# Performance work log

Measured on AMD Instinct MI355X. Metric: run time of the kernel, lower is better.

Reference implementation:

```python
import jax, jax.numpy as jnp
import numpy as np

N_NODES = 50000
N_EDGES = 500000
D_IN = 128
D_HID = 128
D_OUT = 128
N_GRAPHS = 1024


def gcn_conv(x, W, b, row, col, n_nodes):
    # x: [N, d_in] -> [N, d_out]; PyG GCNConv with add_self_loops + symmetric norm
    h = x @ W  # [N, d_out]
    loops = jnp.arange(n_nodes, dtype=row.dtype)
    r = jnp.concatenate([row, loops])  # source
    c = jnp.concatenate([col, loops])  # target
    deg = jax.ops.segment_sum(jnp.ones(r.shape[0], dtype=x.dtype), c, num_segments=n_nodes)
    dinv = jnp.where(deg > 0, jax.lax.rsqrt(jnp.maximum(deg, 1.0)), 0.0)
    norm = dinv[r] * dinv[c]  # [E+N]
    msg = h[r] * norm[:, None]  # gather + scale
    out = jax.ops.segment_sum(msg, c, num_segments=n_nodes)  # scatter-add at targets
    return out + b


def setup_inputs() -> dict:
    key = jax.random.key(0)
    ks = jax.random.split(key, 10)
    x = jax.random.normal(ks[0], (N_NODES, D_IN), dtype=jnp.float32)
    edge_index = jax.random.randint(ks[1], (2, N_EDGES), 0, N_NODES, dtype=jnp.int64)
    batch = jnp.sort(jax.random.randint(ks[2], (N_NODES,), 0, N_GRAPHS, dtype=jnp.int64))
    s1 = 1.0 / np.sqrt(D_IN)
    s2 = 1.0 / np.sqrt(D_HID)
    W1 = jax.random.uniform(ks[3], (D_IN, D_HID), jnp.float32, -s1, s1)
    b1 = jnp.zeros((D_HID,), jnp.float32)
    W2 = jax.random.uniform(ks[4], (D_HID, D_HID), jnp.float32, -s2, s2)
    b2 = jnp.zeros((D_HID,), jnp.float32)
    Wf = jax.random.uniform(ks[5], (D_HID, D_OUT), jnp.float32, -s2, s2)
    bf = jax.random.uniform(ks[6], (D_OUT,), jnp.float32, -s2, s2)
    return {"x": x, "edge_index": edge_index, "batch": batch,
            "W1": W1, "b1": b1, "W2": W2, "b2": b2, "Wf": Wf, "bf": bf}


def reference(x, edge_index, batch, W1, b1, W2, b2, Wf, bf):
    n = x.shape[0]
    row, col = edge_index[0], edge_index[1]
    h = jax.nn.relu(gcn_conv(x, W1, b1, row, col, n))
    h = jax.nn.relu(gcn_conv(h, W2, b2, row, col, n))
    # global_mean_pool over graph ids
    sums = jax.ops.segment_sum(h, batch, num_segments=N_GRAPHS)  # [G, d]
    cnts = jax.ops.segment_sum(jnp.ones((n,), h.dtype), batch, num_segments=N_GRAPHS)
    pooled = sums / jnp.maximum(cnts, 1.0)[:, None]
    return pooled @ Wf + bf  # [G, D_OUT]
```

## Files before the change

### kernel.cpp

```cpp
#include <hip/hip_runtime.h>
#include <hip/hip_bf16.h>


#define D 128

typedef __attribute__((ext_vector_type(8))) short short8;
typedef __attribute__((ext_vector_type(4))) float f32x4;

__device__ __forceinline__ int swz(int row, int kbyte) {
    return row * 256 + (kbyte ^ ((row & 7) << 4));
}

__global__ __launch_bounds__(256) void k_init(int4* __restrict__ degcnt4, int n4, int zb,
                                              const float* __restrict__ W1,
                                              const float* __restrict__ W2,
                                              ushort* __restrict__ h1, ushort* __restrict__ l1,
                                              ushort* __restrict__ h2, ushort* __restrict__ l2) {
    int b = blockIdx.x;
    if (b < zb) {
        int i = b * 256 + threadIdx.x;
        if (i < n4) degcnt4[i] = make_int4(0, 0, 0, 0);
        return;
    }
    int bb = b - zb;
    const float* W = (bb < 8) ? W1 : W2;
    ushort* Wh = (bb < 8) ? h1 : h2;
    ushort* Wl = (bb < 8) ? l1 : l2;
    int t = (bb & 7) * 256 + threadIdx.x;
    int nrow = t >> 4;
    int kc = t & 15;
    uint hw[8], lw[8];
#pragma unroll
    for (int j = 0; j < 8; ++j) {
        float f = W[(kc * 8 + j) * D + nrow];
        uint ub = __float_as_uint(f);
        uint hb = ub & 0xffff0000u;
        float r = f - __uint_as_float(hb);
        hw[j] = hb >> 16;
        lw[j] = __float_as_uint(r) >> 16;
    }
    uint4 vh = make_uint4(hw[0] | (hw[1] << 16), hw[2] | (hw[3] << 16),
                          hw[4] | (hw[5] << 16), hw[6] | (hw[7] << 16));
    uint4 vl = make_uint4(lw[0] | (lw[1] << 16), lw[2] | (lw[3] << 16),
                          lw[4] | (lw[5] << 16), lw[6] | (lw[7] << 16));
    *(uint4*)&Wh[nrow * D + kc * 8] = vh;
    *(uint4*)&Wl[nrow * D + kc * 8] = vl;
}

__global__ void k_deg(const int* __restrict__ col, int* __restrict__ cnt, int E) {
    int e = (blockIdx.x * blockDim.x + threadIdx.x) * 2;
    if (e + 1 < E) {
        int2 c = *(const int2*)&col[e];
        atomicAdd(&cnt[c.x], 1);
        atomicAdd(&cnt[c.y], 1);
    } else if (e < E) {
        atomicAdd(&cnt[col[e]], 1);
    }
}

__global__ __launch_bounds__(256) void k_scan_partial(const int* __restrict__ cnt,
                                                      int* __restrict__ partial, int n) {
    int t = threadIdx.x;
    int base = blockIdx.x * 1024 + t * 4;
    int s = 0;
#pragma unroll
    for (int j = 0; j < 4; ++j) {
        int i = base + j;
        if (i < n) s += cnt[i];
    }
#pragma unroll
    for (int o = 32; o > 0; o >>= 1) s += __shfl_down(s, o, 64);
    __shared__ int ws[4];
    if ((t & 63) == 0) ws[t >> 6] = s;
    __syncthreads();
    if (t == 0) partial[blockIdx.x] = ws[0] + ws[1] + ws[2] + ws[3];
}

__global__ __launch_bounds__(256) void k_scan_final(const int* __restrict__ cnt,
                                                    const int* __restrict__ partial,
                                                    int* __restrict__ offs,
                                                    int* __restrict__ cursor,
                                                    float* __restrict__ dinv,
                                                    int n, int E) {
    int t = threadIdx.x;
    int lane = t & 63;
    int base = blockIdx.x * 1024 + t * 4;
    int v[4];
    int s = 0;
#pragma unroll
    for (int j = 0; j < 4; ++j) {
        int i = base + j;
        v[j] = (i < n) ? cnt[i] : 0;
        s += v[j];
    }
    int inc = s;
#pragma unroll
    for (int o = 1; o < 64; o <<= 1) {
        int u = __shfl_up(inc, o, 64);
        if (lane >= o) inc += u;
    }
    __shared__ int wsum[4];
    __shared__ int bpref;
    if (lane == 63) wsum[t >> 6] = inc;
    if (t == 0) {
        int run = 0;
        for (int b = 0; b < blockIdx.x; ++b) run += partial[b];
        bpref = run;
        if (blockIdx.x == 0) offs[n] = E;
    }
    __syncthreads();
    int woff = 0;
    int w = t >> 6;
    for (int k = 0; k < w; ++k) woff += wsum[k];
    int excl = woff + (inc - s) + bpref;
#pragma unroll
    for (int j = 0; j < 4; ++j) {
        int i = base + j;
        if (i < n) {
            offs[i] = excl;
            cursor[i] = excl;
            dinv[i] = 1.0f / sqrtf((float)(v[j] + 1));
        }
        excl += v[j];
    }
}

__global__ void k_fill(const int* __restrict__ ei, int* __restrict__ cursor,
                       int* __restrict__ csr, int E) {
    int e = (blockIdx.x * blockDim.x + threadIdx.x) * 2;
    if (e + 1 < E) {
        int2 r = *(const int2*)&ei[e];
        int2 c = *(const int2*)&ei[E + e];
        int p0 = atomicAdd(&cursor[c.x], 1);
        csr[p0] = r.x;
        int p1 = atomicAdd(&cursor[c.y], 1);
        csr[p1] = r.y;
    } else if (e < E) {
        int r = ei[e];
        int c = ei[E + e];
        int pos = atomicAdd(&cursor[c], 1);
        csr[pos] = r;
    }
}

#define TM 128
template <bool ASLICED>
__global__ __launch_bounds__(512, 4) void k_gemm(const float* __restrict__ A,
                                                 const ushort* __restrict__ Bt_hi,
                                                 const ushort* __restrict__ Bt_lo,
                                                 const float* __restrict__ dinv,
                                                 float* __restrict__ C, int n) {
    extern __shared__ char lds[];
    char* Bh = lds;
    char* Bl = lds + 32 * 1024;

    int tid = threadIdx.x;
    int wave = tid >> 6, lane = tid & 63;
    int li = lane & 15, lg = lane >> 4;
    int row0 = blockIdx.x * TM;
    int grow = row0 + wave * 16 + li;
    bool valid = grow < n;

    float4 a[4][2];
#pragma unroll
    for (int ks = 0; ks < 4; ++ks) {
        int k0 = ks * 32 + lg * 8;
        if (valid) {
            const float4* p;
            if (ASLICED)
                p = (const float4*)(A + ((size_t)(k0 >> 4) * n + grow) * 16 + (k0 & 15));
            else
                p = (const float4*)(A + (size_t)grow * D + k0);
            a[ks][0] = p[0];
            a[ks][1] = p[1];
        } else {
            a[ks][0] = make_float4(0.f, 0.f, 0.f, 0.f);
            a[ks][1] = make_float4(0.f, 0.f, 0.f, 0.f);
        }
    }

#pragma unroll
    for (int it = tid; it < 2048; it += 512) {
        int r = it >> 4, kc = it & 15;
        uint4 vh = *(const uint4*)(Bt_hi + r * D + kc * 8);
        uint4 vl = *(const uint4*)(Bt_lo + r * D + kc * 8);
        *(uint4*)(Bh + swz(r, kc * 16)) = vh;
        *(uint4*)(Bl + swz(r, kc * 16)) = vl;
    }
    __syncthreads();

    short8 ah[4], al[4];
#pragma unroll
    for (int ks = 0; ks < 4; ++ks) {
        float f[8] = {a[ks][0].x, a[ks][0].y, a[ks][0].z, a[ks][0].w,
                      a[ks][1].x, a[ks][1].y, a[ks][1].z, a[ks][1].w};
#pragma unroll
        for (int j = 0; j < 8; ++j) {
            uint ub = __float_as_uint(f[j]);
            uint hb = ub & 0xffff0000u;
            float r = f[j] - __uint_as_float(hb);
            ah[ks][j] = (short)(hb >> 16);
            al[ks][j] = (short)(__float_as_uint(r) >> 16);
        }
    }

    f32x4 acc[8];
#pragma unroll
    for (int i = 0; i < 8; ++i) acc[i] = (f32x4){0.f, 0.f, 0.f, 0.f};

#pragma unroll
    for (int ks = 0; ks < 4; ++ks) {
        int kb = ks * 64 + lg * 16;
#pragma unroll
        for (int nt = 0; nt < 8; ++nt) {
            short8 bh = *(const short8*)(Bh + swz(nt * 16 + li, kb));
            short8 bl = *(const short8*)(Bl + swz(nt * 16 + li, kb));
            acc[nt] = __builtin_amdgcn_mfma_f32_16x16x32_bf16(ah[ks], bh, acc[nt], 0, 0, 0);
            acc[nt] = __builtin_amdgcn_mfma_f32_16x16x32_bf16(al[ks], bh, acc[nt], 0, 0, 0);
            acc[nt] = __builtin_amdgcn_mfma_f32_16x16x32_bf16(ah[ks], bl, acc[nt], 0, 0, 0);
        }
    }

    int crow0 = row0 + wave * 16 + lg * 4;
#pragma unroll
    for (int j = 0; j < 4; ++j) {
        int gr = crow0 + j;
        if (gr < n) {
            float dv = dinv[gr];
#pragma unroll
            for (int nt = 0; nt < 8; ++nt)
                C[((size_t)nt * n + gr) * 16 + li] = acc[nt][j] * dv;
        }
    }
}

#define AGG_NB 64
__global__ __launch_bounds__(256) void k_agg(const float* __restrict__ hs,
                                             const float* __restrict__ dinv,
                                             const int* __restrict__ offs,
                                             const int* __restrict__ csr,
                                             const float* __restrict__ bias,
                                             float* __restrict__ outs, int n) {
    int slice = blockIdx.x & 7;
    int chunk = blockIdx.x >> 3;
    int node = chunk * AGG_NB + (threadIdx.x >> 2);
    if (node >= n) return;
    int l4 = (threadIdx.x & 3) * 4;

    const float* hbase = hs + (size_t)slice * n * 16;
    float di = dinv[node];
    int s = offs[node], e = offs[node + 1];
    f32x4 acc = *(const f32x4*)(hbase + (size_t)node * 16 + l4);
    int p = s;
    for (; p + 8 <= e; p += 8) {
        int r0 = csr[p],     r1 = csr[p + 1], r2 = csr[p + 2], r3 = csr[p + 3];
        int r4 = csr[p + 4], r5 = csr[p + 5], r6 = csr[p + 6], r7 = csr[p + 7];
        f32x4 h0 = *(const f32x4*)(hbase + (size_t)r0 * 16 + l4);
        f32x4 h1 = *(const f32x4*)(hbase + (size_t)r1 * 16 + l4);
        f32x4 h2 = *(const f32x4*)(hbase + (size_t)r2 * 16 + l4);
        f32x4 h3 = *(const f32x4*)(hbase + (size_t)r3 * 16 + l4);
        f32x4 h4 = *(const f32x4*)(hbase + (size_t)r4 * 16 + l4);
        f32x4 h5 = *(const f32x4*)(hbase + (size_t)r5 * 16 + l4);
        f32x4 h6 = *(const f32x4*)(hbase + (size_t)r6 * 16 + l4);
        f32x4 h7 = *(const f32x4*)(hbase + (size_t)r7 * 16 + l4);
        acc += ((h0 + h1) + (h2 + h3)) + ((h4 + h5) + (h6 + h7));
    }
    for (; p + 4 <= e; p += 4) {
        int r0 = csr[p], r1 = csr[p + 1], r2 = csr[p + 2], r3 = csr[p + 3];
        f32x4 h0 = *(const f32x4*)(hbase + (size_t)r0 * 16 + l4);
        f32x4 h1 = *(const f32x4*)(hbase + (size_t)r1 * 16 + l4);
        f32x4 h2 = *(const f32x4*)(hbase + (size_t)r2 * 16 + l4);
        f32x4 h3 = *(const f32x4*)(hbase + (size_t)r3 * 16 + l4);
        acc += (h0 + h1) + (h2 + h3);
    }
    for (; p < e; ++p) {
        int r = csr[p];
        acc += *(const f32x4*)(hbase + (size_t)r * 16 + l4);
    }
    f32x4 b4 = *(const f32x4*)(bias + slice * 16 + l4);
    f32x4 v;
#pragma unroll
    for (int j = 0; j < 4; ++j) v[j] = fmaxf(acc[j] * di + b4[j], 0.f);
    __builtin_nontemporal_store(v, (f32x4*)(outs + ((size_t)slice * n + node) * 16 + l4));
}

__global__ __launch_bounds__(128) void k_poolfinal(const float* __restrict__ hs,
                                                   const int* __restrict__ batch, int n,
                                                   const float* __restrict__ Wf,
                                                   const float* __restrict__ bf,
                                                   float* __restrict__ out) {
    int g = blockIdx.x;
    int lo = 0, hi = n;
    while (lo < hi) { int m = (lo + hi) >> 1; if (batch[m] < g) lo = m + 1; else hi = m; }
    int s = lo;
    lo = s; hi = n;
    while (lo < hi) { int m = (lo + hi) >> 1; if (batch[m] < g + 1) lo = m + 1; else hi = m; }
    int e = lo;

    int d = threadIdx.x;
    const float* base = hs + (size_t)(d >> 4) * n * 16 + (d & 15);
    float a0 = 0.f, a1 = 0.f, a2 = 0.f, a3 = 0.f;
    int i = s;
    for (; i + 4 <= e; i += 4) {
        a0 += base[(size_t)i * 16];
        a1 += base[(size_t)(i + 1) * 16];
        a2 += base[(size_t)(i + 2) * 16];
        a3 += base[(size_t)(i + 3) * 16];
    }
    for (; i < e; ++i) a0 += base[(size_t)i * 16];
    float acc = (a0 + a1) + (a2 + a3);
    float cnt = (float)(e - s);
    if (cnt < 1.f) cnt = 1.f;

    __shared__ float pr[D];
    pr[d] = acc / cnt;
    __syncthreads();
    float o = bf[d];
#pragma unroll 8
    for (int k = 0; k < D; ++k) o += pr[k] * Wf[k * D + d];
    out[g * D + d] = o;
}

extern "C" void kernel_launch(void* const* d_in, const int* in_sizes, int n_in,
                              void* d_out, int out_size, void* d_ws, size_t ws_size,
                              hipStream_t stream) {
    const float* x  = (const float*)d_in[0];
    const int*   ei = (const int*)d_in[1];
    const int*   bt = (const int*)d_in[2];
    const float* W1 = (const float*)d_in[3];
    const float* b1 = (const float*)d_in[4];
    const float* W2 = (const float*)d_in[5];
    const float* b2 = (const float*)d_in[6];
    const float* Wf = (const float*)d_in[7];
    const float* bf = (const float*)d_in[8];
    float* out = (float*)d_out;

    int n = in_sizes[2];
    int E = in_sizes[1] / 2;
    int G = out_size / D;

    char* w = (char*)d_ws;
    size_t off = 0;
    auto alloc = [&](size_t bytes) -> void* {
        void* p = w + off;
        off = (off + bytes + 511) & ~(size_t)511;
        return p;
    };
    int*    degcnt = (int*)alloc((size_t)n * 4);
    int*    cursor = (int*)alloc((size_t)n * 4);
    int*    offs   = (int*)alloc((size_t)(n + 1) * 4);
    float*  dinv   = (float*)alloc((size_t)n * 4);
    int*    csr    = (int*)alloc((size_t)E * 4);
    float*  hw     = (float*)alloc((size_t)n * D * 4);
    float*  ha     = (float*)alloc((size_t)n * D * 4);
    int*    partial= (int*)alloc((size_t)256 * 4);
    ushort* wt1h   = (ushort*)alloc((size_t)D * D * 2);
    ushort* wt1l   = (ushort*)alloc((size_t)D * D * 2);
    ushort* wt2h   = (ushort*)alloc((size_t)D * D * 2);
    ushort* wt2l   = (ushort*)alloc((size_t)D * D * 2);

    int n4 = (n + 3) / 4;
    int zb = (n4 + 255) / 256;
    k_init<<<zb + 16, 256, 0, stream>>>((int4*)degcnt, n4, zb,
                                        W1, W2, wt1h, wt1l, wt2h, wt2l);

    int e2b = (E / 2 + 255) / 256 + 1;
    int sb = (n + 1023) / 1024;
    k_deg<<<e2b, 256, 0, stream>>>(ei + E, degcnt, E);
    k_scan_partial<<<sb, 256, 0, stream>>>(degcnt, partial, n);
    k_scan_final<<<sb, 256, 0, stream>>>(degcnt, partial, offs, cursor, dinv, n, E);
    k_fill<<<e2b, 256, 0, stream>>>(ei, cursor, csr, E);

    int gb = (n + TM - 1) / TM;
    int ab = 8 * ((n + AGG_NB - 1) / AGG_NB);
    size_t lds_bytes = 64 * 1024;

    k_gemm<false><<<gb, 512, lds_bytes, stream>>>(x, wt1h, wt1l, dinv, hw, n);
    k_agg<<<ab, 256, 0, stream>>>(hw, dinv, offs, csr, b1, ha, n);
    k_gemm<true><<<gb, 512, lds_bytes, stream>>>(ha, wt2h, wt2l, dinv, hw, n);
    k_agg<<<ab, 256, 0, stream>>>(hw, dinv, offs, csr, b2, ha, n);
    k_poolfinal<<<G, 128, 0, stream>>>(ha, bt, n, Wf, bf, out);
}
```

Baseline: 172.9 us.

## Stage CSR slices in LDS for aggregation, widen edge kernels, parallelize pooling

The aggregation kernel now loads each block's offsets and neighbor index range into shared memory once, so the 8 feature-slice blocks no longer each read neighbor indices from global memory per thread. It falls back to global reads when the span exceeds the LDS capacity. The degree and CSR-fill kernels process four edges per thread with int4 loads and issue their atomics together. Pooling splits the binary searches across two threads and reads rows with vector loads spread over four row groups, reduced through shared memory. The cost is extra syncs and LDS use in aggregation.

```diff
diff --git a/kernel.cpp b/kernel.cpp
--- a/kernel.cpp
+++ b/kernel.cpp
@@ -48,13 +48,15 @@
 }
 
 __global__ void k_deg(const int* __restrict__ col, int* __restrict__ cnt, int E) {
-    int e = (blockIdx.x * blockDim.x + threadIdx.x) * 2;
-    if (e + 1 < E) {
-        int2 c = *(const int2*)&col[e];
+    int e = (blockIdx.x * blockDim.x + threadIdx.x) * 4;
+    if (e + 3 < E) {
+        int4 c = *(const int4*)&col[e];
         atomicAdd(&cnt[c.x], 1);
         atomicAdd(&cnt[c.y], 1);
-    } else if (e < E) {
-        atomicAdd(&cnt[col[e]], 1);
+        atomicAdd(&cnt[c.z], 1);
+        atomicAdd(&cnt[c.w], 1);
+    } else {
+        for (; e < E; ++e) atomicAdd(&cnt[col[e]], 1);
     }
 }
 
@@ -127,19 +129,24 @@
 
 __global__ void k_fill(const int* __restrict__ ei, int* __restrict__ cursor,
                        int* __restrict__ csr, int E) {
-    int e = (blockIdx.x * blockDim.x + threadIdx.x) * 2;
-    if (e + 1 < E) {
-        int2 r = *(const int2*)&ei[e];
-        int2 c = *(const int2*)&ei[E + e];
+    int e = (blockIdx.x * blockDim.x + threadIdx.x) * 4;
+    if (e + 3 < E) {
+        int4 r = *(const int4*)&ei[e];
+        int4 c = *(const int4*)&ei[E + e];
         int p0 = atomicAdd(&cursor[c.x], 1);
+        int p1 = atomicAdd(&cursor[c.y], 1);
+        int p2 = atomicAdd(&cursor[c.z], 1);
+        int p3 = atomicAdd(&cursor[c.w], 1);
         csr[p0] = r.x;
-        int p1 = atomicAdd(&cursor[c.y], 1);
         csr[p1] = r.y;
-    } else if (e < E) {
-        int r = ei[e];
-        int c = ei[E + e];
-        int pos = atomicAdd(&cursor[c], 1);
-        csr[pos] = r;
+        csr[p2] = r.z;
+        csr[p3] = r.w;
+    } else {
+        for (; e < E; ++e) {
+            int rr = ei[e], cc = ei[E + e];
+            int pos = atomicAdd(&cursor[cc], 1);
+            csr[pos] = rr;
+        }
     }
 }
 
@@ -235,47 +242,77 @@
 }
 
 #define AGG_NB 64
+#define CSR_CAP 1152
 __global__ __launch_bounds__(256) void k_agg(const float* __restrict__ hs,
                                              const float* __restrict__ dinv,
                                              const int* __restrict__ offs,
                                              const int* __restrict__ csr,
                                              const float* __restrict__ bias,
                                              float* __restrict__ outs, int n) {
+    __shared__ int lofs[AGG_NB + 1];
+    __shared__ int lcsr[CSR_CAP];
     int slice = blockIdx.x & 7;
     int chunk = blockIdx.x >> 3;
-    int node = chunk * AGG_NB + (threadIdx.x >> 2);
+    int node0 = chunk * AGG_NB;
+    int nend = node0 + AGG_NB; if (nend > n) nend = n;
+    int nn = nend - node0;
+    if (threadIdx.x <= nn) lofs[threadIdx.x] = offs[node0 + threadIdx.x];
+    __syncthreads();
+    int S = lofs[0];
+    int span = lofs[nn] - S;
+    bool uselds = (span <= CSR_CAP);
+    if (uselds) {
+        for (int i = threadIdx.x; i < span; i += 256) lcsr[i] = csr[S + i];
+    }
+    __syncthreads();
+
+    int lnode = threadIdx.x >> 2;
+    int node = node0 + lnode;
     if (node >= n) return;
     int l4 = (threadIdx.x & 3) * 4;
 
     const float* hbase = hs + (size_t)slice * n * 16;
     float di = dinv[node];
-    int s = offs[node], e = offs[node + 1];
+    int s = lofs[lnode] - S, e = lofs[lnode + 1] - S;
     f32x4 acc = *(const f32x4*)(hbase + (size_t)node * 16 + l4);
-    int p = s;
-    for (; p + 8 <= e; p += 8) {
-        int r0 = csr[p],     r1 = csr[p + 1], r2 = csr[p + 2], r3 = csr[p + 3];
-        int r4 = csr[p + 4], r5 = csr[p + 5], r6 = csr[p + 6], r7 = csr[p + 7];
-        f32x4 h0 = *(const f32x4*)(hbase + (size_t)r0 * 16 + l4);
-        f32x4 h1 = *(const f32x4*)(hbase + (size_t)r1 * 16 + l4);
-        f32x4 h2 = *(const f32x4*)(hbase + (size_t)r2 * 16 + l4);
-        f32x4 h3 = *(const f32x4*)(hbase + (size_t)r3 * 16 + l4);
-        f32x4 h4 = *(const f32x4*)(hbase + (size_t)r4 * 16 + l4);
-        f32x4 h5 = *(const f32x4*)(hbase + (size_t)r5 * 16 + l4);
-        f32x4 h6 = *(const f32x4*)(hbase + (size_t)r6 * 16 + l4);
-        f32x4 h7 = *(const f32x4*)(hbase + (size_t)r7 * 16 + l4);
-        acc += ((h0 + h1) + (h2 + h3)) + ((h4 + h5) + (h6 + h7));
-    }
-    for (; p + 4 <= e; p += 4) {
-        int r0 = csr[p], r1 = csr[p + 1], r2 = csr[p + 2], r3 = csr[p + 3];
-        f32x4 h0 = *(const f32x4*)(hbase + (size_t)r0 * 16 + l4);
-        f32x4 h1 = *(const f32x4*)(hbase + (size_t)r1 * 16 + l4);
-        f32x4 h2 = *(const f32x4*)(hbase + (size_t)r2 * 16 + l4);
-        f32x4 h3 = *(const f32x4*)(hbase + (size_t)r3 * 16 + l4);
-        acc += (h0 + h1) + (h2 + h3);
-    }
-    for (; p < e; ++p) {
-        int r = csr[p];
-        acc += *(const f32x4*)(hbase + (size_t)r * 16 + l4);
+    if (uselds) {
+        int p = s;
+        for (; p + 8 <= e; p += 8) {
+            int r0 = lcsr[p],     r1 = lcsr[p + 1], r2 = lcsr[p + 2], r3 = lcsr[p + 3];
+            int r4 = lcsr[p + 4], r5 = lcsr[p + 5], r6 = lcsr[p + 6], r7 = lcsr[p + 7];
+            f32x4 h0 = *(const f32x4*)(hbase + (size_t)r0 * 16 + l4);
+            f32x4 h1 = *(const f32x4*)(hbase + (size_t)r1 * 16 + l4);
+            f32x4 h2 = *(const f32x4*)(hbase + (size_t)r2 * 16 + l4);
+            f32x4 h3 = *(const f32x4*)(hbase + (size_t)r3 * 16 + l4);
+            f32x4 h4 = *(const f32x4*)(hbase + (size_t)r4 * 16 + l4);
+            f32x4 h5 = *(const f32x4*)(hbase + (size_t)r5 * 16 + l4);
+            f32x4 h6 = *(const f32x4*)(hbase + (size_t)r6 * 16 + l4);
+            f32x4 h7 = *(const f32x4*)(hbase + (size_t)r7 * 16 + l4);
+            acc += ((h0 + h1) + (h2 + h3)) + ((h4 + h5) + (h6 + h7));
+        }
+        for (; p + 4 <= e; p += 4) {
+            int r0 = lcsr[p], r1 = lcsr[p + 1], r2 = lcsr[p + 2], r3 = lcsr[p + 3];
+            f32x4 h0 = *(const f32x4*)(hbase + (size_t)r0 * 16 + l4);
+            f32x4 h1 = *(const f32x4*)(hbase + (size_t)r1 * 16 + l4);
+            f32x4 h2 = *(const f32x4*)(hbase + (size_t)r2 * 16 + l4);
+            f32x4 h3 = *(const f32x4*)(hbase + (size_t)r3 * 16 + l4);
+            acc += (h0 + h1) + (h2 + h3);
+        }
+        for (; p < e; ++p)
+            acc += *(const f32x4*)(hbase + (size_t)lcsr[p] * 16 + l4);
+    } else {
+        const int* gcsr = csr + S;
+        int p = s;
+        for (; p + 4 <= e; p += 4) {
+            int r0 = gcsr[p], r1 = gcsr[p + 1], r2 = gcsr[p + 2], r3 = gcsr[p + 3];
+            f32x4 h0 = *(const f32x4*)(hbase + (size_t)r0 * 16 + l4);
+            f32x4 h1 = *(const f32x4*)(hbase + (size_t)r1 * 16 + l4);
+            f32x4 h2 = *(const f32x4*)(hbase + (size_t)r2 * 16 + l4);
+            f32x4 h3 = *(const f32x4*)(hbase + (size_t)r3 * 16 + l4);
+            acc += (h0 + h1) + (h2 + h3);
+        }
+        for (; p < e; ++p)
+            acc += *(const f32x4*)(hbase + (size_t)gcsr[p] * 16 + l4);
     }
     f32x4 b4 = *(const f32x4*)(bias + slice * 16 + l4);
     f32x4 v;
@@ -289,32 +326,42 @@
                                                    const float* __restrict__ Wf,
                                                    const float* __restrict__ bf,
                                                    float* __restrict__ out) {
+    __shared__ int sse[2];
     int g = blockIdx.x;
-    int lo = 0, hi = n;
-    while (lo < hi) { int m = (lo + hi) >> 1; if (batch[m] < g) lo = m + 1; else hi = m; }
-    int s = lo;
-    lo = s; hi = n;
-    while (lo < hi) { int m = (lo + hi) >> 1; if (batch[m] < g + 1) lo = m + 1; else hi = m; }
-    int e = lo;
-
+    if (threadIdx.x == 0) {
+        int lo = 0, hi = n;
+        while (lo < hi) { int m = (lo + hi) >> 1; if (batch[m] < g) lo = m + 1; else hi = m; }
+        sse[0] = lo;
+    } else if (threadIdx.x == 64) {
+        int lo = 0, hi = n;
+        while (lo < hi) { int m = (lo + hi) >> 1; if (batch[m] < g + 1) lo = m + 1; else hi = m; }
+        sse[1] = lo;
+    }
+    __syncthreads();
+    int s = sse[0], e = sse[1];
+
+    int q = threadIdx.x & 31;
+    int r = threadIdx.x >> 5;
+    int slice = q >> 2;
+    int l4 = (q & 3) * 4;
+    const float* base = hs + (size_t)slice * n * 16 + l4;
+    f32x4 acc = (f32x4){0.f, 0.f, 0.f, 0.f};
+    for (int i = s + r; i < e; i += 4)
+        acc += *(const f32x4*)(base + (size_t)i * 16);
+
+    __shared__ f32x4 red[128];
+    __shared__ float pr[D];
+    red[threadIdx.x] = acc;
+    __syncthreads();
+    if (threadIdx.x < 32) {
+        f32x4 t = (red[q] + red[q + 32]) + (red[q + 64] + red[q + 96]);
+        float cnt = (float)(e - s);
+        if (cnt < 1.f) cnt = 1.f;
+#pragma unroll
+        for (int j = 0; j < 4; ++j) pr[q * 4 + j] = t[j] / cnt;
+    }
+    __syncthreads();
     int d = threadIdx.x;
-    const float* base = hs + (size_t)(d >> 4) * n * 16 + (d & 15);
-    float a0 = 0.f, a1 = 0.f, a2 = 0.f, a3 = 0.f;
-    int i = s;
-    for (; i + 4 <= e; i += 4) {
-        a0 += base[(size_t)i * 16];
-        a1 += base[(size_t)(i + 1) * 16];
-        a2 += base[(size_t)(i + 2) * 16];
-        a3 += base[(size_t)(i + 3) * 16];
-    }
-    for (; i < e; ++i) a0 += base[(size_t)i * 16];
-    float acc = (a0 + a1) + (a2 + a3);
-    float cnt = (float)(e - s);
-    if (cnt < 1.f) cnt = 1.f;
-
-    __shared__ float pr[D];
-    pr[d] = acc / cnt;
-    __syncthreads();
     float o = bf[d];
 #pragma unroll 8
     for (int k = 0; k < D; ++k) o += pr[k] * Wf[k * D + d];
@@ -364,12 +411,12 @@
     k_init<<<zb + 16, 256, 0, stream>>>((int4*)degcnt, n4, zb,
                                         W1, W2, wt1h, wt1l, wt2h, wt2l);
 
-    int e2b = (E / 2 + 255) / 256 + 1;
+    int e4b = (E / 4 + 255) / 256 + 1;
     int sb = (n + 1023) / 1024;
-    k_deg<<<e2b, 256, 0, stream>>>(ei + E, degcnt, E);
+    k_deg<<<e4b, 256, 0, stream>>>(ei + E, degcnt, E);
     k_scan_partial<<<sb, 256, 0, stream>>>(degcnt, partial, n);
     k_scan_final<<<sb, 256, 0, stream>>>(degcnt, partial, offs, cursor, dinv, n, E);
-    k_fill<<<e2b, 256, 0, stream>>>(ei, cursor, csr, E);
+    k_fill<<<e4b, 256, 0, stream>>>(ei, cursor, csr, E);
 
     int gb = (n + TM - 1) / TM;
     int ab = 8 * ((n + AGG_NB - 1) / AGG_NB);
```

After: 164.5 us. 1.05x faster.
